# Kernel tuning notes

Hardware: AMD Instinct MI355X
Metric: run time of the kernel (lower is better)

## Reference

```python
import jax, jax.numpy as jnp
import numpy as np

N = 100000
E = 1600000
F_IN = 128
HID = 16
HEADS = 8
NCLS = 2
NGRAPH = 64
NEG_SLOPE = 0.2


def setup_inputs() -> dict:
    key = jax.random.key(0)
    ks = jax.random.split(key, 12)
    x = jax.random.normal(ks[0], (N, F_IN), dtype=jnp.float32)
    edge_index = jax.random.randint(ks[1], (2, E), 0, N, dtype=jnp.int64)
    batch = jnp.sort(jax.random.randint(ks[2], (N,), 0, NGRAPH, dtype=jnp.int64))
    s1 = 1.0 / np.sqrt(F_IN)
    s2 = 1.0 / np.sqrt(HEADS * HID)
    W1 = jax.random.normal(ks[3], (F_IN, HEADS * HID), dtype=jnp.float32) * s1
    att_src1 = jax.random.normal(ks[4], (HEADS, HID), dtype=jnp.float32) * s2
    att_dst1 = jax.random.normal(ks[5], (HEADS, HID), dtype=jnp.float32) * s2
    b1 = jnp.zeros((HEADS * HID,), dtype=jnp.float32)
    W2 = jax.random.normal(ks[6], (HEADS * HID, 1 * NCLS), dtype=jnp.float32) * s2
    att_src2 = jax.random.normal(ks[7], (1, NCLS), dtype=jnp.float32)
    att_dst2 = jax.random.normal(ks[8], (1, NCLS), dtype=jnp.float32)
    b2 = jnp.zeros((NCLS,), dtype=jnp.float32)
    return {"x": x, "edge_index": edge_index, "batch": batch,
            "W1": W1, "att_src1": att_src1, "att_dst1": att_dst1, "b1": b1,
            "W2": W2, "att_src2": att_src2, "att_dst2": att_dst2, "b2": b2}


def _gat_conv(x, src, dst, W, att_src, att_dst, bias, heads, out_dim, concat):
    # x: [N, Fin]; src/dst: [E'] (self-loops already appended)
    h = (x @ W).reshape(N, heads, out_dim)              # [N, H, D]
    a_src = jnp.sum(h * att_src[None], axis=-1)          # [N, H]
    a_dst = jnp.sum(h * att_dst[None], axis=-1)          # [N, H]
    e = a_src[src] + a_dst[dst]                          # [E', H]
    e = jnp.where(e >= 0, e, NEG_SLOPE * e)              # leaky_relu
    # softmax over incoming edges of each destination node
    emax = jax.ops.segment_max(e, dst, num_segments=N)   # [N, H]
    ee = jnp.exp(e - emax[dst])
    denom = jax.ops.segment_sum(ee, dst, num_segments=N)
    alpha = ee / denom[dst]                              # [E', H]
    msg = h[src] * alpha[:, :, None]                     # [E', H, D]
    out = jax.ops.segment_sum(msg, dst, num_segments=N)  # [N, H, D]
    if concat:
        out = out.reshape(N, heads * out_dim)
    else:
        out = out.mean(axis=1)
    return out + bias


def reference(x, edge_index, batch, W1, att_src1, att_dst1, b1, W2, att_src2, att_dst2, b2):
    # add self-loops (PyG GATConv default add_self_loops=True)
    loop = jnp.arange(N, dtype=edge_index.dtype)
    src = jnp.concatenate([edge_index[0], loop])
    dst = jnp.concatenate([edge_index[1], loop])

    h = _gat_conv(x, src, dst, W1, att_src1, att_dst1, b1, HEADS, HID, True)
    h = jax.nn.elu(h)
    h = _gat_conv(h, src, dst, W2, att_src2, att_dst2, b2, 1, NCLS, False)

    # global mean pool over graphs
    ssum = jax.ops.segment_sum(h, batch, num_segments=NGRAPH)          # [G, C]
    cnt = jax.ops.segment_sum(jnp.ones((N,), h.dtype), batch, num_segments=NGRAPH)
    pooled = ssum / jnp.maximum(cnt, 1.0)[:, None]
    return jax.nn.log_softmax(pooled, axis=1)
```

## Files before the change

### kernel.cpp

```cpp
#include <hip/hip_runtime.h>
#include <math.h>

typedef long long ll;
typedef unsigned int u32;
typedef unsigned short u16;
typedef __attribute__((ext_vector_type(8))) short short8;
typedef __attribute__((ext_vector_type(4))) float f32x4;

#define NBLK 256
#define MAXBUK 512
#define CHUNK_MAX 8192

__device__ __forceinline__ int load_idx(const void* p, int i, int is64) {
  return is64 ? (int)((const ll*)p)[i] : ((const int*)p)[i];
}

__device__ __forceinline__ u16 f2bf(float f) {
  u32 u = __float_as_uint(f);
  u += 0x7FFFu + ((u >> 16) & 1u);
  return (u16)(u >> 16);
}

__global__ __launch_bounds__(256) void prep_kernel(
    const void* __restrict__ eidx, int ne2, const void* __restrict__ batch, int nb,
    const float* __restrict__ W1, u16* __restrict__ Wtb,
    float* __restrict__ pool, int* __restrict__ flags) {
  int blk = blockIdx.x, t = threadIdx.x;
  if (blk < 64) {
    int g = blk * 256 + t;
    int k = g >> 7, j = g & 127;
    Wtb[j * 128 + k] = f2bf(W1[g]);
  } else {
    if (t < 192) pool[t] = 0.f;
    ll v = 0;
    if (t < 16) {
      int i = (int)((ll)(t + 1) * (ne2 / 2 - 1) / 16);
      v = ((const ll*)eidx)[i];
    } else if (t < 32) {
      int i = (int)((ll)(t - 15) * (nb / 2 - 1) / 16);
      v = ((const ll*)batch)[i];
    }
    bool bad = (v < 0 || v >= (1LL << 31));
    unsigned long long mask = __ballot(bad);
    if (t == 0) {
      flags[0] = (mask & 0xFFFFull) ? 0 : 1;
      flags[1] = (mask & 0xFFFF0000ull) ? 0 : 1;
    }
  }
}

__global__ __launch_bounds__(256) void gemm1_kernel(
    const float* __restrict__ x, const u16* __restrict__ Wtb,
    const float* __restrict__ att_src, const float* __restrict__ att_dst,
    u16* __restrict__ h, float* __restrict__ a_src, float* __restrict__ a_dst,
    int nn) {
  __shared__ __align__(16) char smem[64 * 136 * 2 + 128 * 136 * 2];
  u16* xs = (u16*)smem;
  u16* Wt = (u16*)(smem + 64 * 136 * 2);
  float* hs = (float*)smem;
  int t = threadIdx.x;
  int n0 = blockIdx.x * 64;

  const uint4* W4 = (const uint4*)Wtb;
  #pragma unroll
  for (int p = 0; p < 8; ++p) {
    int i = t + p * 256;
    int j = i >> 4, kc = (i & 15) * 8;
    *(uint4*)&Wt[j * 136 + kc] = W4[i];
  }
  #pragma unroll
  for (int p = 0; p < 4; ++p) {
    int row = p * 16 + (t >> 4);
    int c = t & 15;
    int gn = n0 + row;
    uint4 pk = make_uint4(0u, 0u, 0u, 0u);
    if (gn < nn) {
      const float4* xp = (const float4*)(x + (size_t)gn * 128 + c * 8);
      float4 f0 = xp[0], f1 = xp[1];
      pk.x = (u32)f2bf(f0.x) | ((u32)f2bf(f0.y) << 16);
      pk.y = (u32)f2bf(f0.z) | ((u32)f2bf(f0.w) << 16);
      pk.z = (u32)f2bf(f1.x) | ((u32)f2bf(f1.y) << 16);
      pk.w = (u32)f2bf(f1.z) | ((u32)f2bf(f1.w) << 16);
    }
    *(uint4*)&xs[row * 136 + c * 8] = pk;
  }
  __syncthreads();

  int lane = t & 63, wid = t >> 6;
  int lrow = lane & 15, lq = lane >> 4;
  short8 a[4];
  #pragma unroll
  for (int ks = 0; ks < 4; ++ks) {
    int row = wid * 16 + lrow;
    a[ks] = *(const short8*)&xs[row * 136 + ks * 32 + lq * 8];
  }
  f32x4 c[8];
  #pragma unroll
  for (int jt = 0; jt < 8; ++jt) c[jt] = (f32x4)(0.f);
  #pragma unroll
  for (int jt = 0; jt < 8; ++jt) {
    int j = jt * 16 + lrow;
    #pragma unroll
    for (int ks = 0; ks < 4; ++ks) {
      short8 b = *(const short8*)&Wt[j * 136 + ks * 32 + lq * 8];
      c[jt] = __builtin_amdgcn_mfma_f32_16x16x32_bf16(a[ks], b, c[jt], 0, 0, 0);
    }
  }
  __syncthreads();

  #pragma unroll
  for (int jt = 0; jt < 8; ++jt) {
    #pragma unroll
    for (int r = 0; r < 4; ++r) {
      hs[(wid * 16 + lq * 4 + r) * 132 + jt * 16 + lrow] = c[jt][r];
    }
  }
  __syncthreads();

  int q = t & 31, p = t >> 5;
  const float4 as4 = ((const float4*)att_src)[q];
  const float4 ad4 = ((const float4*)att_dst)[q];
  int head = q >> 2;
  #pragma unroll
  for (int rr = 0; rr < 8; ++rr) {
    int row = rr * 8 + p;
    int n = n0 + row;
    float4 v = *(const float4*)&hs[row * 132 + q * 4];
    float s = v.x * as4.x + v.y * as4.y + v.z * as4.z + v.w * as4.w;
    float d = v.x * ad4.x + v.y * ad4.y + v.z * ad4.z + v.w * ad4.w;
    s += __shfl_xor(s, 1); s += __shfl_xor(s, 2);
    d += __shfl_xor(d, 1); d += __shfl_xor(d, 2);
    if (n < nn) {
      uint2 pk;
      pk.x = (u32)f2bf(v.x) | ((u32)f2bf(v.y) << 16);
      pk.y = (u32)f2bf(v.z) | ((u32)f2bf(v.w) << 16);
      ((uint2*)(h + (size_t)n * 128))[q] = pk;
      if ((q & 3) == 0) { a_src[n * 8 + head] = s; a_dst[n * 8 + head] = d; }
    }
  }
}

__global__ __launch_bounds__(512) void ehist_kernel(
    const void* __restrict__ eidx, int E, int EP, int chunk,
    const int* __restrict__ flags, int* __restrict__ hist_g, int nbuk) {
  __shared__ int cnt[MAXBUK];
  int t = threadIdx.x, blk = blockIdx.x;
  if (t < MAXBUK) cnt[t] = 0;
  __syncthreads();
  int lo = blk * chunk, hi = min(lo + chunk, EP);
  int is64 = flags[0];
  for (int i = lo + t; i < hi; i += 512) {
    int d = (i < E) ? load_idx(eidx, E + i, is64) : (i - E);
    atomicAdd(&cnt[d >> 8], 1);
  }
  __syncthreads();
  if (t < nbuk) hist_g[t * NBLK + blk] = cnt[t];
}

__global__ __launch_bounds__(256) void scan_blk(const int* __restrict__ in,
                                                int* __restrict__ out,
                                                int* __restrict__ bsums, int n) {
  int t = threadIdx.x;
  int i = blockIdx.x * 256 + t;
  int v = (i < n) ? in[i] : 0;
  int lane = t & 63, w = t >> 6;
  int s = v;
  #pragma unroll
  for (int off = 1; off < 64; off <<= 1) {
    int u = __shfl_up(s, off);
    if (lane >= off) s += u;
  }
  __shared__ int wsum[4];
  if (lane == 63) wsum[w] = s;
  __syncthreads();
  int add = 0;
  for (int k = 0; k < w; ++k) add += wsum[k];
  int incl = s + add;
  if (i < n) out[i] = incl - v;
  if (t == 255) bsums[blockIdx.x] = incl;
}

__global__ __launch_bounds__(1024) void scan_top(int* __restrict__ bsums, int nb) {
  int t = threadIdx.x;
  int v = (t < nb) ? bsums[t] : 0;
  int lane = t & 63, w = t >> 6;
  int s = v;
  #pragma unroll
  for (int off = 1; off < 64; off <<= 1) {
    int u = __shfl_up(s, off);
    if (lane >= off) s += u;
  }
  __shared__ int ws[16];
  if (lane == 63) ws[w] = s;
  __syncthreads();
  int add = 0;
  for (int k = 0; k < w; ++k) add += ws[k];
  if (t < nb) bsums[t] = s + add - v;
}

__global__ __launch_bounds__(512) void escatter_kernel(
    const void* __restrict__ eidx, int E, int EP, int chunk,
    const int* __restrict__ flags, const int* __restrict__ hist_g,
    const int* __restrict__ pbase, const int* __restrict__ bsums,
    u32* __restrict__ pairs, int nbuk) {
  __shared__ int cnt[MAXBUK];
  __shared__ int lbase[MAXBUK];
  __shared__ int lcur[MAXBUK];
  __shared__ u32 buf[CHUNK_MAX];
  __shared__ int wsum[8];
  int t = threadIdx.x, blk = blockIdx.x;
  int v = 0;
  if (t < nbuk) { v = hist_g[t * NBLK + blk]; cnt[t] = v; }
  int lane = t & 63, w = t >> 6;
  int s = v;
  #pragma unroll
  for (int off = 1; off < 64; off <<= 1) {
    int u = __shfl_up(s, off);
    if (lane >= off) s += u;
  }
  if (lane == 63) wsum[w] = s;
  __syncthreads();
  int add = 0;
  for (int k = 0; k < w; ++k) add += wsum[k];
  if (t < nbuk) { lbase[t] = s + add - v; lcur[t] = s + add - v; }
  __syncthreads();
  int lo = blk * chunk, hi = min(lo + chunk, EP);
  int is64 = flags[0];
  for (int i = lo + t; i < hi; i += 512) {
    int sv, d;
    if (i < E) { sv = load_idx(eidx, i, is64); d = load_idx(eidx, E + i, is64); }
    else { sv = d = i - E; }
    int pos = atomicAdd(&lcur[d >> 8], 1);
    buf[pos] = ((u32)(d & 255) << 24) | (u32)sv;
  }
  __syncthreads();
  for (int b = w; b < nbuk; b += 8) {
    int n_b = cnt[b];
    int lb = lbase[b];
    int gb = pbase[b * NBLK + blk] + bsums[b];
    for (int k = lane; k < n_b; k += 64) {
      pairs[gb + k] = buf[lb + k];
    }
  }
}

__global__ __launch_bounds__(256) void bfinal_kernel(
    const u32* __restrict__ pairs, const int* __restrict__ pbase,
    const int* __restrict__ bsums,
    int* __restrict__ offs, int* __restrict__ ends, int* __restrict__ ssrc,
    int N, int EP, int nbuk) {
  int b = blockIdx.x, t = threadIdx.x;
  int nb0 = b << 8;
  __shared__ int cnt[256];
  __shared__ int cur[256];
  __shared__ int wsum[4];
  cnt[t] = 0;
  __syncthreads();
  int seg_start = pbase[b * NBLK] + bsums[b];
  int seg_end = (b + 1 < nbuk) ? (pbase[(b + 1) * NBLK] + bsums[b + 1]) : EP;
  for (int i = seg_start + t; i < seg_end; i += 256) {
    atomicAdd(&cnt[pairs[i] >> 24], 1);
  }
  __syncthreads();
  int v = cnt[t];
  int lane = t & 63, w = t >> 6;
  int s = v;
  #pragma unroll
  for (int off = 1; off < 64; off <<= 1) {
    int u = __shfl_up(s, off);
    if (lane >= off) s += u;
  }
  if (lane == 63) wsum[w] = s;
  __syncthreads();
  int add = 0;
  for (int k = 0; k < w; ++k) add += wsum[k];
  int excl = s + add - v;
  cur[t] = excl;
  int node = nb0 + t;
  if (node < N) { offs[node] = seg_start + excl; ends[node] = seg_start + excl + v; }
  __syncthreads();
  for (int i = seg_start + t; i < seg_end; i += 256) {
    u32 p = pairs[i];
    int pos = atomicAdd(&cur[p >> 24], 1);
    ssrc[seg_start + pos] = (int)(p & 0xFFFFFFu);
  }
}

__global__ __launch_bounds__(256) void node1_kernel(
    const int* __restrict__ ssrc, const int* __restrict__ offs, const int* __restrict__ ends,
    const u16* __restrict__ h, const float* __restrict__ a_src, const float* __restrict__ a_dst,
    const float* __restrict__ b1, const float* __restrict__ W2,
    const float* __restrict__ att_s2, const float* __restrict__ att_d2,
    float4* __restrict__ rec, int nn) {
  int t = threadIdx.x;
  int wid = t >> 6, lane = t & 63;
  int grp = lane >> 4, lg = lane & 15;
  int n = blockIdx.x * 16 + wid * 4 + grp;
  bool nvalid = (n < nn);
  int nc = nvalid ? n : (nn - 1);
  int hh = lg >> 1;
  float adst = a_dst[nc * 8 + hh];
  int beg = offs[nc], end = ends[nc];
  int deg = nvalid ? (end - beg) : 0;
  int maxd = deg;
  maxd = max(maxd, __shfl_xor(maxd, 16));
  maxd = max(maxd, __shfl_xor(maxd, 32));
  float acc[8];
  #pragma unroll
  for (int k = 0; k < 8; ++k) acc[k] = 0.f;
  float dsum = 0.f;
  const u32* h32 = (const u32*)h;
  for (int it = 0; it < maxd; it += 4) {
    int s4[4]; float ea4[4]; uint4 v4[4];
    #pragma unroll
    for (int u = 0; u < 4; ++u) {
      int id = beg + it + u;
      s4[u] = ssrc[id < end ? id : end - 1];
    }
    #pragma unroll
    for (int u = 0; u < 4; ++u) {
      v4[u]  = *(const uint4*)(h32 + s4[u] * 64 + lg * 4);
      ea4[u] = a_src[s4[u] * 8 + hh];
    }
    #pragma unroll
    for (int u = 0; u < 4; ++u) {
      float e = ea4[u] + adst;
      e = fmaxf(e, 0.2f * e);
      float ee = (it + u < deg) ? __expf(e) : 0.f;
      dsum += ee;
      acc[0] = fmaf(ee, __uint_as_float(v4[u].x << 16),          acc[0]);
      acc[1] = fmaf(ee, __uint_as_float(v4[u].x & 0xFFFF0000u),  acc[1]);
      acc[2] = fmaf(ee, __uint_as_float(v4[u].y << 16),          acc[2]);
      acc[3] = fmaf(ee, __uint_as_float(v4[u].y & 0xFFFF0000u),  acc[3]);
      acc[4] = fmaf(ee, __uint_as_float(v4[u].z << 16),          acc[4]);
      acc[5] = fmaf(ee, __uint_as_float(v4[u].z & 0xFFFF0000u),  acc[5]);
      acc[6] = fmaf(ee, __uint_as_float(v4[u].w << 16),          acc[6]);
      acc[7] = fmaf(ee, __uint_as_float(v4[u].w & 0xFFFF0000u),  acc[7]);
    }
  }
  float inv = 1.f / dsum;
  float p0 = 0.f, p1 = 0.f;
  #pragma unroll
  for (int k = 0; k < 8; ++k) {
    int j = lg * 8 + k;
    float o = acc[k] * inv + b1[j];
    o = (o > 0.f) ? o : expm1f(o);
    p0 = fmaf(o, W2[j * 2],     p0);
    p1 = fmaf(o, W2[j * 2 + 1], p1);
  }
  #pragma unroll
  for (int m = 1; m < 16; m <<= 1) { p0 += __shfl_xor(p0, m); p1 += __shfl_xor(p1, m); }
  if (nvalid && lg == 0) {
    rec[n] = make_float4(p0, p1,
                         p0 * att_s2[0] + p1 * att_s2[1],
                         p0 * att_d2[0] + p1 * att_d2[1]);
  }
}

__global__ __launch_bounds__(256) void node2_kernel(
    const int* __restrict__ ssrc, const int* __restrict__ offs, const int* __restrict__ ends,
    const float4* __restrict__ rec, const float* __restrict__ b2,
    const void* __restrict__ batch, const int* __restrict__ flags,
    float* __restrict__ pool, int nn) {
  __shared__ float psum[128];
  __shared__ float pcnt[64];
  int t = threadIdx.x;
  if (t < 128) psum[t] = 0.f;
  if (t < 64) pcnt[t] = 0.f;
  __syncthreads();
  int grp = t >> 3, lane8 = t & 7;
  int b64 = flags[1];
  int n = blockIdx.x * 32 + grp;
  if (n < nn) {
    float adst = rec[n].w;
    int beg = offs[n], end = ends[n];
    float acc0 = 0.f, acc1 = 0.f, dsum = 0.f;
    for (int idx = beg + lane8; idx < end; idx += 8) {
      int s = ssrc[idx];
      float4 r = rec[s];
      float e = r.z + adst;
      e = (e < 0.f) ? 0.2f * e : e;
      float ee = __expf(e);
      acc0 = fmaf(ee, r.x, acc0);
      acc1 = fmaf(ee, r.y, acc1);
      dsum += ee;
    }
    #pragma unroll
    for (int m = 1; m < 8; m <<= 1) {
      acc0 += __shfl_xor(acc0, m);
      acc1 += __shfl_xor(acc1, m);
      dsum += __shfl_xor(dsum, m);
    }
    if (lane8 == 0) {
      float o0 = acc0 / dsum + b2[0];
      float o1 = acc1 / dsum + b2[1];
      int g = load_idx(batch, n, b64);
      atomicAdd(&psum[g * 2], o0);
      atomicAdd(&psum[g * 2 + 1], o1);
      atomicAdd(&pcnt[g], 1.f);
    }
  }
  __syncthreads();
  if (t < 64 && pcnt[t] > 0.f) {
    atomicAdd(&pool[t * 2], psum[t * 2]);
    atomicAdd(&pool[t * 2 + 1], psum[t * 2 + 1]);
    atomicAdd(&pool[128 + t], pcnt[t]);
  }
}

__global__ void finalize_kernel(const float* __restrict__ pool, float* __restrict__ out) {
  int g = threadIdx.x;
  if (g < 64) {
    float c = fmaxf(pool[128 + g], 1.f);
    float p0 = pool[g * 2] / c, p1 = pool[g * 2 + 1] / c;
    float m = fmaxf(p0, p1);
    float lse = m + logf(expf(p0 - m) + expf(p1 - m));
    out[g * 2] = p0 - lse;
    out[g * 2 + 1] = p1 - lse;
  }
}

extern "C" void kernel_launch(void* const* d_in, const int* in_sizes, int n_in,
                              void* d_out, int out_size, void* d_ws, size_t ws_size,
                              hipStream_t stream) {
  const float* x        = (const float*)d_in[0];
  const void* eidx      = d_in[1];
  const void* batch     = d_in[2];
  const float* W1       = (const float*)d_in[3];
  const float* att_src1 = (const float*)d_in[4];
  const float* att_dst1 = (const float*)d_in[5];
  const float* b1       = (const float*)d_in[6];
  const float* W2       = (const float*)d_in[7];
  const float* att_src2 = (const float*)d_in[8];
  const float* att_dst2 = (const float*)d_in[9];
  const float* b2       = (const float*)d_in[10];
  float* out = (float*)d_out;

  int N = in_sizes[0] / 128;
  int E = in_sizes[1] / 2;
  int EP = E + N;
  int NBUK = (N + 255) >> 8;
  int NC = NBUK * NBLK;
  int chunk = (((EP + NBLK - 1) / NBLK) + 1) & ~1;

  char* ws = (char*)d_ws;
  size_t o = 0;
  auto alloc = [&](size_t bytes) -> void* {
    void* p = ws + o;
    o += (bytes + 255) & ~(size_t)255;
    return p;
  };
  u16*   h      = (u16*)alloc((size_t)N * 128 * 2);
  u16*   Wtb    = (u16*)alloc(128 * 128 * 2);
  float* a_src1 = (float*)alloc((size_t)N * 8 * 4);
  float* a_dst1 = (float*)alloc((size_t)N * 8 * 4);
  int*   offs   = (int*)alloc((size_t)N * 4);
  int*   ends   = (int*)alloc((size_t)N * 4);
  int*   hist_g = (int*)alloc((size_t)NC * 4);
  int*   pbase  = (int*)alloc((size_t)NC * 4);
  int*   bsums  = (int*)alloc((size_t)(NBUK + 1) * 4);
  u32*   pairs  = (u32*)alloc((size_t)EP * 4);
  int*   ssrc   = (int*)alloc((size_t)EP * 4);
  float4* rec   = (float4*)alloc((size_t)N * 16);
  float* pool   = (float*)alloc(192 * 4);
  int*   flags  = (int*)alloc(2 * 4);

  prep_kernel<<<65, 256, 0, stream>>>(eidx, 2 * E, batch, N, W1, Wtb, pool, flags);
  gemm1_kernel<<<(N + 63) / 64, 256, 0, stream>>>(x, Wtb, att_src1, att_dst1,
                                                  h, a_src1, a_dst1, N);
  ehist_kernel<<<NBLK, 512, 0, stream>>>(eidx, E, EP, chunk, flags, hist_g, NBUK);
  scan_blk<<<NBUK, 256, 0, stream>>>(hist_g, pbase, bsums, NC);
  scan_top<<<1, 1024, 0, stream>>>(bsums, NBUK);
  escatter_kernel<<<NBLK, 512, 0, stream>>>(eidx, E, EP, chunk, flags, hist_g,
                                            pbase, bsums, pairs, NBUK);
  bfinal_kernel<<<NBUK, 256, 0, stream>>>(pairs, pbase, bsums, offs, ends, ssrc,
                                          N, EP, NBUK);
  node1_kernel<<<(N + 15) / 16, 256, 0, stream>>>(ssrc, offs, ends, h, a_src1, a_dst1,
                                                  b1, W2, att_src2, att_dst2,
                                                  rec, N);
  node2_kernel<<<(N + 31) / 32, 256, 0, stream>>>(ssrc, offs, ends, rec,
                                                  b2, batch, flags, pool, N);
  finalize_kernel<<<1, 64, 0, stream>>>(pool, out);
}
```

Baseline: 205.0 us.

## Sort nodes by degree for balanced aggregation, widen edge-sort blocks, prefetch sources

Adds a counting sort of nodes by in-degree bucket (histogram, scan, scatter kernels) so node1 processes nodes of similar degree in the same wavefront, which cuts idle lanes caused by the per-wave max-degree loop. It also doubles the number of edge-sorting blocks, halves the chunk size, widens scan_blk and bfinal to 512 threads, and software-prefetches the next four source indices in node1. The cost is three extra small launches, an indirection through perm, and reads of h/a_dst/offs that are less coalesced for permuted nodes.

Result: slower. 217.3 us (+6.0%).

```diff
diff --git a/kernel.cpp b/kernel.cpp
--- a/kernel.cpp
+++ b/kernel.cpp
@@ -7,9 +7,9 @@
 typedef __attribute__((ext_vector_type(8))) short short8;
 typedef __attribute__((ext_vector_type(4))) float f32x4;
 
-#define NBLK 256
+#define NBLK 512
 #define MAXBUK 512
-#define CHUNK_MAX 8192
+#define CHUNK_MAX 4096
 
 __device__ __forceinline__ int load_idx(const void* p, int i, int is64) {
   return is64 ? (int)((const ll*)p)[i] : ((const int*)p)[i];
@@ -24,7 +24,7 @@
 __global__ __launch_bounds__(256) void prep_kernel(
     const void* __restrict__ eidx, int ne2, const void* __restrict__ batch, int nb,
     const float* __restrict__ W1, u16* __restrict__ Wtb,
-    float* __restrict__ pool, int* __restrict__ flags) {
+    float* __restrict__ pool, int* __restrict__ gbin, int* __restrict__ flags) {
   int blk = blockIdx.x, t = threadIdx.x;
   if (blk < 64) {
     int g = blk * 256 + t;
@@ -32,6 +32,7 @@
     Wtb[j * 128 + k] = f2bf(W1[g]);
   } else {
     if (t < 192) pool[t] = 0.f;
+    if (t < 64) gbin[t] = 0;
     ll v = 0;
     if (t < 16) {
       int i = (int)((ll)(t + 1) * (ne2 / 2 - 1) / 16);
@@ -157,12 +158,12 @@
   if (t < nbuk) hist_g[t * NBLK + blk] = cnt[t];
 }
 
-__global__ __launch_bounds__(256) void scan_blk(const int* __restrict__ in,
+__global__ __launch_bounds__(512) void scan_blk(const int* __restrict__ in,
                                                 int* __restrict__ out,
-                                                int* __restrict__ bsums, int n) {
-  int t = threadIdx.x;
-  int i = blockIdx.x * 256 + t;
-  int v = (i < n) ? in[i] : 0;
+                                                int* __restrict__ bsums, int nc) {
+  int t = threadIdx.x;
+  int i = blockIdx.x * NBLK + t;
+  int v = (i < nc) ? in[i] : 0;
   int lane = t & 63, w = t >> 6;
   int s = v;
   #pragma unroll
@@ -170,14 +171,14 @@
     int u = __shfl_up(s, off);
     if (lane >= off) s += u;
   }
-  __shared__ int wsum[4];
+  __shared__ int wsum[8];
   if (lane == 63) wsum[w] = s;
   __syncthreads();
   int add = 0;
   for (int k = 0; k < w; ++k) add += wsum[k];
   int incl = s + add;
-  if (i < n) out[i] = incl - v;
-  if (t == 255) bsums[blockIdx.x] = incl;
+  if (i < nc) out[i] = incl - v;
+  if (t == NBLK - 1) bsums[blockIdx.x] = incl;
 }
 
 __global__ __launch_bounds__(1024) void scan_top(int* __restrict__ bsums, int nb) {
@@ -244,7 +245,7 @@
   }
 }
 
-__global__ __launch_bounds__(256) void bfinal_kernel(
+__global__ __launch_bounds__(512) void bfinal_kernel(
     const u32* __restrict__ pairs, const int* __restrict__ pbase,
     const int* __restrict__ bsums,
     int* __restrict__ offs, int* __restrict__ ends, int* __restrict__ ssrc,
@@ -253,16 +254,16 @@
   int nb0 = b << 8;
   __shared__ int cnt[256];
   __shared__ int cur[256];
-  __shared__ int wsum[4];
-  cnt[t] = 0;
+  __shared__ int wsum[8];
+  if (t < 256) cnt[t] = 0;
   __syncthreads();
   int seg_start = pbase[b * NBLK] + bsums[b];
   int seg_end = (b + 1 < nbuk) ? (pbase[(b + 1) * NBLK] + bsums[b + 1]) : EP;
-  for (int i = seg_start + t; i < seg_end; i += 256) {
+  for (int i = seg_start + t; i < seg_end; i += 512) {
     atomicAdd(&cnt[pairs[i] >> 24], 1);
   }
   __syncthreads();
-  int v = cnt[t];
+  int v = (t < 256) ? cnt[t] : 0;
   int lane = t & 63, w = t >> 6;
   int s = v;
   #pragma unroll
@@ -275,18 +276,70 @@
   int add = 0;
   for (int k = 0; k < w; ++k) add += wsum[k];
   int excl = s + add - v;
-  cur[t] = excl;
-  int node = nb0 + t;
-  if (node < N) { offs[node] = seg_start + excl; ends[node] = seg_start + excl + v; }
-  __syncthreads();
-  for (int i = seg_start + t; i < seg_end; i += 256) {
+  if (t < 256) {
+    cur[t] = excl;
+    int node = nb0 + t;
+    if (node < N) { offs[node] = seg_start + excl; ends[node] = seg_start + excl + v; }
+  }
+  __syncthreads();
+  for (int i = seg_start + t; i < seg_end; i += 512) {
     u32 p = pairs[i];
     int pos = atomicAdd(&cur[p >> 24], 1);
     ssrc[seg_start + pos] = (int)(p & 0xFFFFFFu);
   }
 }
 
+__global__ __launch_bounds__(256) void dhist_kernel(
+    const int* __restrict__ offs, const int* __restrict__ ends,
+    int* __restrict__ gbin, int N) {
+  __shared__ int lb[64];
+  int t = threadIdx.x;
+  if (t < 64) lb[t] = 0;
+  __syncthreads();
+  int i = blockIdx.x * 256 + t;
+  if (i < N) {
+    int b = min((ends[i] - offs[i]) >> 2, 63);
+    atomicAdd(&lb[b], 1);
+  }
+  __syncthreads();
+  if (t < 64 && lb[t]) atomicAdd(&gbin[t], lb[t]);
+}
+
+__global__ __launch_bounds__(64) void dscan_kernel(const int* __restrict__ gbin,
+                                                   int* __restrict__ gcur) {
+  int t = threadIdx.x;
+  int v = gbin[t];
+  int s = v;
+  #pragma unroll
+  for (int off = 1; off < 64; off <<= 1) {
+    int u = __shfl_up(s, off);
+    if (t >= off) s += u;
+  }
+  gcur[t] = s - v;
+}
+
+__global__ __launch_bounds__(256) void dscatter_kernel(
+    const int* __restrict__ offs, const int* __restrict__ ends,
+    int* __restrict__ gcur, int* __restrict__ perm, int N) {
+  __shared__ int lb[64];
+  __shared__ int lbase[64];
+  int t = threadIdx.x;
+  if (t < 64) lb[t] = 0;
+  __syncthreads();
+  int i = blockIdx.x * 256 + t;
+  int b = 0, pos = 0;
+  if (i < N) {
+    b = min((ends[i] - offs[i]) >> 2, 63);
+    pos = atomicAdd(&lb[b], 1);
+  }
+  __syncthreads();
+  if (t < 64 && lb[t]) lbase[t] = atomicAdd(&gcur[t], lb[t]);
+  __syncthreads();
+  if (i < N) perm[lbase[b] + pos] = i;
+}
+
 __global__ __launch_bounds__(256) void node1_kernel(
+    const int* __restrict__ perm,
     const int* __restrict__ ssrc, const int* __restrict__ offs, const int* __restrict__ ends,
     const u16* __restrict__ h, const float* __restrict__ a_src, const float* __restrict__ a_dst,
     const float* __restrict__ b1, const float* __restrict__ W2,
@@ -295,12 +348,12 @@
   int t = threadIdx.x;
   int wid = t >> 6, lane = t & 63;
   int grp = lane >> 4, lg = lane & 15;
-  int n = blockIdx.x * 16 + wid * 4 + grp;
-  bool nvalid = (n < nn);
-  int nc = nvalid ? n : (nn - 1);
+  int nidx = blockIdx.x * 16 + wid * 4 + grp;
+  bool nvalid = (nidx < nn);
+  int n = perm[nvalid ? nidx : 0];
   int hh = lg >> 1;
-  float adst = a_dst[nc * 8 + hh];
-  int beg = offs[nc], end = ends[nc];
+  float adst = a_dst[n * 8 + hh];
+  int beg = offs[n], end = ends[n];
   int deg = nvalid ? (end - beg) : 0;
   int maxd = deg;
   maxd = max(maxd, __shfl_xor(maxd, 16));
@@ -310,13 +363,20 @@
   for (int k = 0; k < 8; ++k) acc[k] = 0.f;
   float dsum = 0.f;
   const u32* h32 = (const u32*)h;
+
+  int s4[4], ns4[4];
+  #pragma unroll
+  for (int u = 0; u < 4; ++u) {
+    int id = beg + u;
+    s4[u] = ssrc[id < end ? id : (end - 1)];
+  }
   for (int it = 0; it < maxd; it += 4) {
-    int s4[4]; float ea4[4]; uint4 v4[4];
     #pragma unroll
     for (int u = 0; u < 4; ++u) {
-      int id = beg + it + u;
-      s4[u] = ssrc[id < end ? id : end - 1];
-    }
+      int id = beg + it + 4 + u;
+      ns4[u] = ssrc[id < end ? id : (end - 1)];
+    }
+    float ea4[4]; uint4 v4[4];
     #pragma unroll
     for (int u = 0; u < 4; ++u) {
       v4[u]  = *(const uint4*)(h32 + s4[u] * 64 + lg * 4);
@@ -337,6 +397,8 @@
       acc[6] = fmaf(ee, __uint_as_float(v4[u].w << 16),          acc[6]);
       acc[7] = fmaf(ee, __uint_as_float(v4[u].w & 0xFFFF0000u),  acc[7]);
     }
+    #pragma unroll
+    for (int u = 0; u < 4; ++u) s4[u] = ns4[u];
   }
   float inv = 1.f / dsum;
   float p0 = 0.f, p1 = 0.f;
@@ -461,23 +523,29 @@
   int*   bsums  = (int*)alloc((size_t)(NBUK + 1) * 4);
   u32*   pairs  = (u32*)alloc((size_t)EP * 4);
   int*   ssrc   = (int*)alloc((size_t)EP * 4);
+  int*   perm   = (int*)alloc((size_t)N * 4);
+  int*   gbin   = (int*)alloc(64 * 4);
+  int*   gcur   = (int*)alloc(64 * 4);
   float4* rec   = (float4*)alloc((size_t)N * 16);
   float* pool   = (float*)alloc(192 * 4);
   int*   flags  = (int*)alloc(2 * 4);
 
-  prep_kernel<<<65, 256, 0, stream>>>(eidx, 2 * E, batch, N, W1, Wtb, pool, flags);
+  prep_kernel<<<65, 256, 0, stream>>>(eidx, 2 * E, batch, N, W1, Wtb, pool, gbin, flags);
   gemm1_kernel<<<(N + 63) / 64, 256, 0, stream>>>(x, Wtb, att_src1, att_dst1,
                                                   h, a_src1, a_dst1, N);
   ehist_kernel<<<NBLK, 512, 0, stream>>>(eidx, E, EP, chunk, flags, hist_g, NBUK);
-  scan_blk<<<NBUK, 256, 0, stream>>>(hist_g, pbase, bsums, NC);
+  scan_blk<<<NBUK, 512, 0, stream>>>(hist_g, pbase, bsums, NC);
   scan_top<<<1, 1024, 0, stream>>>(bsums, NBUK);
   escatter_kernel<<<NBLK, 512, 0, stream>>>(eidx, E, EP, chunk, flags, hist_g,
                                             pbase, bsums, pairs, NBUK);
-  bfinal_kernel<<<NBUK, 256, 0, stream>>>(pairs, pbase, bsums, offs, ends, ssrc,
+  bfinal_kernel<<<NBUK, 512, 0, stream>>>(pairs, pbase, bsums, offs, ends, ssrc,
                                           N, EP, NBUK);
-  node1_kernel<<<(N + 15) / 16, 256, 0, stream>>>(ssrc, offs, ends, h, a_src1, a_dst1,
-                                                  b1, W2, att_src2, att_dst2,
-                                                  rec, N);
+  dhist_kernel<<<(N + 255) / 256, 256, 0, stream>>>(offs, ends, gbin, N);
+  dscan_kernel<<<1, 64, 0, stream>>>(gbin, gcur);
+  dscatter_kernel<<<(N + 255) / 256, 256, 0, stream>>>(offs, ends, gcur, perm, N);
+  node1_kernel<<<(N + 15) / 16, 256, 0, stream>>>(perm, ssrc, offs, ends, h,
+                                                  a_src1, a_dst1, b1, W2,
+                                                  att_src2, att_dst2, rec, N);
   node2_kernel<<<(N + 31) / 32, 256, 0, stream>>>(ssrc, offs, ends, rec,
                                                   b2, batch, flags, pool, N);
   finalize_kernel<<<1, 64, 0, stream>>>(pool, out);
```
